# Performance work log

Measured on AMD Instinct MI355X. Metric: run time of the kernel, lower is better.

The kernel has to match this reference:

```python
import jax, jax.numpy as jnp
import numpy as np

H = 4096
W = 4096
C = 3
OUT = 1024
MAX_MIP = 8  # matches init max_mip_level; mip chain is levels 0..MAX_MIP


def setup_inputs() -> dict:
    key = jax.random.key(0)
    k1, k2, k3 = jax.random.split(key, 3)
    data = jax.random.uniform(k1, (1, H, W, C), dtype=jnp.float32)
    texc = jax.random.uniform(k2, (1, OUT, OUT, 2), dtype=jnp.float32)
    # small UV derivatives -> per-pixel texel footprint of a few texels, so the
    # LOD spans several mip levels (exercises cross-level paged gathers)
    texc_deriv = jax.random.normal(k3, (1, OUT, OUT, 4), dtype=jnp.float32) * 2e-3
    return {"data": data, "texc": texc, "texc_deriv": texc_deriv}


def _avg_pool2(x):
    # 2x2 box-filter mipmap reduction, matching virtual_texture_mipmap_fwd
    b, h, w, c = x.shape
    return x.reshape(b, h // 2, 2, w // 2, 2, c).mean(axis=(2, 4))


def _bilinear_wrap(tex, texc):
    # tex: [1,h,w,c]; texc: [1,Ho,Wo,2] in [0,1); boundary_mode='wrap'
    h, w = tex.shape[1], tex.shape[2]
    x = texc[..., 0] * w - 0.5
    y = texc[..., 1] * h - 0.5
    x0f = jnp.floor(x)
    y0f = jnp.floor(y)
    fx = (x - x0f)[..., None]
    fy = (y - y0f)[..., None]
    x0 = x0f.astype(jnp.int32) % w
    y0 = y0f.astype(jnp.int32) % h
    x1 = (x0 + 1) % w
    y1 = (y0 + 1) % h
    t = tex[0]  # [h,w,c]
    top = t[y0, x0] * (1.0 - fx) + t[y0, x1] * fx
    bot = t[y1, x0] * (1.0 - fx) + t[y1, x1] * fx
    return top * (1.0 - fy) + bot * fy  # [1,Ho,Wo,c]


def _forward(data, texc, texc_deriv):
    # LOD from screen-space UV derivatives (nvdiffrast linear-mipmap-linear)
    dudx = texc_deriv[..., 0] * W
    dvdx = texc_deriv[..., 1] * H
    dudy = texc_deriv[..., 2] * W
    dvdy = texc_deriv[..., 3] * H
    rho2 = jnp.maximum(dudx * dudx + dvdx * dvdx, dudy * dudy + dvdy * dvdy)
    lod = 0.5 * jnp.log2(jnp.maximum(rho2, 1e-20))
    lod = jnp.clip(lod, 0.0, float(MAX_MIP))  # [1,Ho,Wo]

    # build mip pyramid (gradients flow back to base texture, matching
    # virtual_texture_mipmap_bwd accumulation)
    mips = [data]
    for _ in range(MAX_MIP):
        mips.append(_avg_pool2(mips[-1]))

    # trilinear: per-level weight w_l = clip(1 - |lod - l|, 0, 1)
    out = jnp.zeros(texc.shape[:-1] + (C,), dtype=data.dtype)
    for lvl in range(MAX_MIP + 1):
        w_l = jnp.clip(1.0 - jnp.abs(lod - float(lvl)), 0.0, 1.0)[..., None]
        out = out + w_l * _bilinear_wrap(mips[lvl], texc)
    return out


def reference(data, texc, texc_deriv):
    return _forward(data, texc, texc_deriv)
```

## Files before the change

### kernel.cpp

```cpp
#include <hip/hip_runtime.h>
#include <hip/hip_bf16.h>


#define OUT_N (1024 * 1024)

__device__ __forceinline__ unsigned mip_off_b(int lvl) {
    return (67108864u - (67108864u >> (2 * lvl - 2))) / 3u;
}
#define OFF2 16777216u
#define OFF3 20971520u
#define OFF4 22020096u
#define OFF5 22282240u
#define OFF6 22347776u

__device__ __forceinline__ unsigned pack10(float r, float g, float b) {
    unsigned ur = __float2uint_rn(r * 1023.0f);
    unsigned ug = __float2uint_rn(g * 1023.0f);
    unsigned ub = __float2uint_rn(b * 1023.0f);
    return ur | (ug << 10) | (ub << 20);
}

__device__ __forceinline__ void dec_acc(unsigned q, float w, float& r, float& g, float& b) {
    const float s = 1.0f / 1023.0f;
    r = fmaf((float)(q & 1023u) * s, w, r);
    g = fmaf((float)((q >> 10) & 1023u) * s, w, g);
    b = fmaf((float)((q >> 20) & 1023u) * s, w, b);
}

__device__ __forceinline__ float4 dec4(unsigned q) {
    const float s = 1.0f / 1023.0f;
    return float4{(float)(q & 1023u) * s, (float)((q >> 10) & 1023u) * s,
                  (float)((q >> 20) & 1023u) * s, 0.0f};
}

__device__ __forceinline__ float4 avg4(float4 a, float4 b, float4 c, float4 d) {
    return float4{(a.x + b.x + c.x + d.x) * 0.25f,
                  (a.y + b.y + c.y + d.y) * 0.25f,
                  (a.z + b.z + c.z + d.z) * 0.25f, 0.0f};
}

__device__ __forceinline__ void store_quad(char* p, float4 t00, float4 t01,
                                           float4 t10, float4 t11) {
    *(uint4*)p = make_uint4(pack10(t00.x, t00.y, t00.z), pack10(t01.x, t01.y, t01.z),
                            pack10(t10.x, t10.y, t10.z), pack10(t11.x, t11.y, t11.z));
}

#define POOL_BYTES (49152 + 4352)

__global__ __launch_bounds__(256) void mip_fused(const float* __restrict__ data,
                                                 char* __restrict__ wsb) {
    __shared__ float4 pool4[POOL_BYTES / 16];
    char* pool = (char*)pool4;
    float4(*s2)[17] = (float4(*)[17])(pool + 49152);
    float4(*s3)[9]  = (float4(*)[9])(pool + 0);
    float4(*s4)[5]  = (float4(*)[5])(pool + 2048);
    float4(*s5)[3]  = (float4(*)[3])(pool + 4096);

    const int t = threadIdx.x;
    const int bx = blockIdx.x & 63;
    const int by = blockIdx.x >> 6;

    {
        const char* src = (const char*)data + (size_t)by * 64 * 49152 + (size_t)bx * 768;
#pragma unroll
        for (int j = 0; j < 12; ++j) {
            int f = t + j * 256;
            int row = f / 48;
            int col = f - row * 48;
            const char* g = src + (size_t)row * 49152 + (size_t)col * 16;
            __builtin_amdgcn_global_load_lds(
                (const __attribute__((address_space(1))) unsigned int*)g,
                (__attribute__((address_space(3))) unsigned int*)(pool + (size_t)f * 16),
                16, 0, 0);
        }
    }
    __syncthreads();

    {
        int tx = t & 15, ty = t >> 4;
        float rr = 0.0f, gg = 0.0f, bb = 0.0f;
#pragma unroll
        for (int i = 0; i < 4; ++i) {
            const float4* rp = (const float4*)(pool + (size_t)(4 * ty + i) * 768 + (size_t)tx * 48);
            float4 A = rp[0], Bv = rp[1], Cv = rp[2];
            rr += A.x + A.w + Bv.z + Cv.y;
            gg += A.y + Bv.x + Bv.w + Cv.z;
            bb += A.z + Bv.y + Cv.x + Cv.w;
        }
        const float sc = 1.0f / 16.0f;
        float4 tex = {rr * sc, gg * sc, bb * sc, 0.0f};
        __syncthreads();
        s2[ty][tx] = tex;
    }
    __syncthreads();

    if (t < 64) {
        int qx = t & 7, qy = t >> 3;
        float4 t00 = s2[2 * qy][2 * qx],     t01 = s2[2 * qy][2 * qx + 1];
        float4 t10 = s2[2 * qy + 1][2 * qx], t11 = s2[2 * qy + 1][2 * qx + 1];
        unsigned gq = ((by << 3) + qy) * 512u + (bx << 3) + qx;
        store_quad(wsb + OFF2 + ((size_t)gq << 4), t00, t01, t10, t11);
        s3[qy][qx] = avg4(t00, t01, t10, t11);
    }
    __syncthreads();

    if (t < 16) {
        int qx = t & 3, qy = t >> 2;
        float4 t00 = s3[2 * qy][2 * qx],     t01 = s3[2 * qy][2 * qx + 1];
        float4 t10 = s3[2 * qy + 1][2 * qx], t11 = s3[2 * qy + 1][2 * qx + 1];
        unsigned gq = ((by << 2) + qy) * 256u + (bx << 2) + qx;
        store_quad(wsb + OFF3 + ((size_t)gq << 4), t00, t01, t10, t11);
        s4[qy][qx] = avg4(t00, t01, t10, t11);
    }
    __syncthreads();

    if (t < 4) {
        int qx = t & 1, qy = t >> 1;
        float4 t00 = s4[2 * qy][2 * qx],     t01 = s4[2 * qy][2 * qx + 1];
        float4 t10 = s4[2 * qy + 1][2 * qx], t11 = s4[2 * qy + 1][2 * qx + 1];
        unsigned gq = ((by << 1) + qy) * 128u + (bx << 1) + qx;
        store_quad(wsb + OFF4 + ((size_t)gq << 4), t00, t01, t10, t11);
        s5[qy][qx] = avg4(t00, t01, t10, t11);
    }
    __syncthreads();

    if (t == 0) {
        float4 t00 = s5[0][0], t01 = s5[0][1], t10 = s5[1][0], t11 = s5[1][1];
        unsigned gq = (unsigned)by * 64u + (unsigned)bx;
        store_quad(wsb + OFF5 + ((size_t)gq << 4), t00, t01, t10, t11);
        float4 l6 = avg4(t00, t01, t10, t11);
        size_t a6 = OFF6 + ((((by >> 1) * 32) + (bx >> 1)) << 4) +
                    ((by & 1) << 3) + ((bx & 1) << 2);
        *(unsigned*)(wsb + a6) = pack10(l6.x, l6.y, l6.z);
    }
}

__device__ __forceinline__ void tap_off(int lvl, float u, float v,
                                        unsigned& o00, unsigned& o01,
                                        unsigned& o10, unsigned& o11,
                                        float& fx, float& fy) {
    int size = 4096 >> lvl;
    float fs = (float)size;
    float x = fmaf(u, fs, -0.5f);
    float y = fmaf(v, fs, -0.5f);
    float x0f = floorf(x);
    float y0f = floorf(y);
    fx = x - x0f;
    fy = y - y0f;
    int m = size - 1;
    int x0 = ((int)x0f) & m;
    int y0 = ((int)y0f) & m;
    int x1 = (x0 + 1) & m;
    int y1 = (y0 + 1) & m;
    int hs = size >> 1;
    unsigned r0 = (unsigned)((y0 >> 1) * hs);
    unsigned r1 = (unsigned)((y1 >> 1) * hs);
    unsigned c0 = (unsigned)(x0 >> 1), c1 = (unsigned)(x1 >> 1);
    unsigned sy0 = (unsigned)((y0 & 1) << 3), sy1 = (unsigned)((y1 & 1) << 3);
    unsigned sx0 = (unsigned)((x0 & 1) << 2), sx1 = (unsigned)((x1 & 1) << 2);
    o00 = ((r0 + c0) << 4) + sy0 + sx0;
    o01 = ((r0 + c1) << 4) + sy0 + sx1;
    o10 = ((r1 + c0) << 4) + sy1 + sx0;
    o11 = ((r1 + c1) << 4) + sy1 + sx1;
}

__device__ __forceinline__ void sample_packed(const char* __restrict__ wsb, int lvl,
                                              float u, float v, float wgt,
                                              float& r, float& g, float& b) {
    unsigned o00, o01, o10, o11;
    float fx, fy;
    tap_off(lvl, u, v, o00, o01, o10, o11, fx, fy);
    const char* B = wsb + mip_off_b(lvl);
    unsigned q00 = *(const unsigned*)(B + o00);
    unsigned q01 = *(const unsigned*)(B + o01);
    unsigned q10 = *(const unsigned*)(B + o10);
    unsigned q11 = *(const unsigned*)(B + o11);
    dec_acc(q00, (1.0f - fx) * (1.0f - fy) * wgt, r, g, b);
    dec_acc(q01, fx * (1.0f - fy) * wgt, r, g, b);
    dec_acc(q10, (1.0f - fx) * fy * wgt, r, g, b);
    dec_acc(q11, fx * fy * wgt, r, g, b);
}

__device__ void sample_fine(const float* __restrict__ data, int lvl,
                            float u, float v, float wgt,
                            float& r, float& g, float& b) {
    int size = 4096 >> lvl;
    float fs = (float)size;
    float x = u * fs - 0.5f;
    float y = v * fs - 0.5f;
    float x0f = floorf(x);
    float y0f = floorf(y);
    float fx = x - x0f;
    float fy = y - y0f;
    int m = size - 1;
    int x0 = ((int)x0f) & m;
    int y0 = ((int)y0f) & m;
    int x1 = (x0 + 1) & m;
    int y1 = (y0 + 1) & m;
    int k = 1 << lvl;
    float inv = wgt / (float)(k * k);
    float ww[2][2] = {{(1.0f - fx) * (1.0f - fy) * inv, fx * (1.0f - fy) * inv},
                      {(1.0f - fx) * fy * inv, fx * fy * inv}};
    int xs[2] = {x0 << lvl, x1 << lvl};
    int ys[2] = {y0 << lvl, y1 << lvl};
    for (int ty = 0; ty < 2; ++ty)
        for (int tx = 0; tx < 2; ++tx) {
            float tr = 0.0f, tg = 0.0f, tb = 0.0f;
            for (int dy = 0; dy < k; ++dy)
                for (int dx = 0; dx < k; ++dx) {
                    const float* p = data + ((size_t)(ys[ty] + dy) * 4096 + xs[tx] + dx) * 3;
                    tr += p[0]; tg += p[1]; tb += p[2];
                }
            r = fmaf(tr, ww[ty][tx], r);
            g = fmaf(tg, ww[ty][tx], g);
            b = fmaf(tb, ww[ty][tx], b);
        }
}

__device__ float4 read_l6(const char* __restrict__ wsb, int xx, int yy) {
    size_t a = OFF6 + ((((yy >> 1) * 32) + (xx >> 1)) << 4) + ((yy & 1) << 3) + ((xx & 1) << 2);
    return dec4(*(const unsigned*)(wsb + a));
}

__device__ void sample_coarse(const char* __restrict__ wsb, int lvl,
                              float u, float v, float wgt,
                              float& r, float& g, float& b) {
    int size = 4096 >> lvl;
    float fs = (float)size;
    float x = u * fs - 0.5f;
    float y = v * fs - 0.5f;
    float x0f = floorf(x);
    float y0f = floorf(y);
    float fx = x - x0f;
    float fy = y - y0f;
    int m = size - 1;
    int x0 = ((int)x0f) & m;
    int y0 = ((int)y0f) & m;
    int x1 = (x0 + 1) & m;
    int y1 = (y0 + 1) & m;
    int s = lvl - 6;
    int k = 1 << s;
    float inv = wgt / (float)(k * k);
    float ww[2][2] = {{(1.0f - fx) * (1.0f - fy) * inv, fx * (1.0f - fy) * inv},
                      {(1.0f - fx) * fy * inv, fx * fy * inv}};
    int xs[2] = {x0 << s, x1 << s};
    int ys[2] = {y0 << s, y1 << s};
    for (int ty = 0; ty < 2; ++ty)
        for (int tx = 0; tx < 2; ++tx) {
            float tr = 0.0f, tg = 0.0f, tb = 0.0f;
            for (int dy = 0; dy < k; ++dy)
                for (int dx = 0; dx < k; ++dx) {
                    float4 c = read_l6(wsb, xs[tx] + dx, ys[ty] + dy);
                    tr += c.x; tg += c.y; tb += c.z;
                }
            r = fmaf(tr, ww[ty][tx], r);
            g = fmaf(tg, ww[ty][tx], g);
            b = fmaf(tb, ww[ty][tx], b);
        }
}

__device__ __forceinline__ void sample_any(const float* __restrict__ data,
                                           const char* __restrict__ wsb, int lvl,
                                           float u, float v, float wgt,
                                           float& r, float& g, float& b) {
    if (lvl >= 2) {
        if (lvl <= 6) sample_packed(wsb, lvl, u, v, wgt, r, g, b);
        else sample_coarse(wsb, lvl, u, v, wgt, r, g, b);
    } else {
        sample_fine(data, lvl, u, v, wgt, r, g, b);
    }
}

__global__ __launch_bounds__(256) void vt_sample(const float* __restrict__ data,
                                                 const char* __restrict__ wsb,
                                                 const float* __restrict__ texc,
                                                 const float* __restrict__ deriv,
                                                 float* __restrict__ out) {
    int p = blockIdx.x * 256 + threadIdx.x;

    float2 uv = ((const float2*)texc)[p];
    float4 dv = ((const float4*)deriv)[p];
    float dudx = dv.x * 4096.0f;
    float dvdx = dv.y * 4096.0f;
    float dudy = dv.z * 4096.0f;
    float dvdy = dv.w * 4096.0f;
    float rho2 = fmaxf(fmaf(dudx, dudx, dvdx * dvdx), fmaf(dudy, dudy, dvdy * dvdy));
    float lod = 0.5f * __log2f(fmaxf(rho2, 1e-20f));
    lod = fminf(fmaxf(lod, 0.0f), 8.0f);

    int l0 = (int)lod;
    float f = lod - (float)l0;
    int l1 = (l0 < 8) ? (l0 + 1) : 8;

    float r = 0.0f, g = 0.0f, b = 0.0f;

    if (__builtin_expect((unsigned)(l0 - 2) <= 3u, 1)) {
        unsigned a00, a01, a10, a11, b00, b01, b10, b11;
        float fx0, fy0, fx1, fy1;
        const char* B0 = wsb + mip_off_b(l0);
        const char* B1 = wsb + mip_off_b(l1);
        tap_off(l0, uv.x, uv.y, a00, a01, a10, a11, fx0, fy0);
        tap_off(l1, uv.x, uv.y, b00, b01, b10, b11, fx1, fy1);
        unsigned q0 = *(const unsigned*)(B0 + a00);
        unsigned q1 = *(const unsigned*)(B0 + a01);
        unsigned q2 = *(const unsigned*)(B0 + a10);
        unsigned q3 = *(const unsigned*)(B0 + a11);
        unsigned q4 = *(const unsigned*)(B1 + b00);
        unsigned q5 = *(const unsigned*)(B1 + b01);
        unsigned q6 = *(const unsigned*)(B1 + b10);
        unsigned q7 = *(const unsigned*)(B1 + b11);
        float w0 = 1.0f - f;
        dec_acc(q0, (1.0f - fx0) * (1.0f - fy0) * w0, r, g, b);
        dec_acc(q1, fx0 * (1.0f - fy0) * w0, r, g, b);
        dec_acc(q2, (1.0f - fx0) * fy0 * w0, r, g, b);
        dec_acc(q3, fx0 * fy0 * w0, r, g, b);
        dec_acc(q4, (1.0f - fx1) * (1.0f - fy1) * f, r, g, b);
        dec_acc(q5, fx1 * (1.0f - fy1) * f, r, g, b);
        dec_acc(q6, (1.0f - fx1) * fy1 * f, r, g, b);
        dec_acc(q7, fx1 * fy1 * f, r, g, b);
    } else {
        sample_any(data, wsb, l0, uv.x, uv.y, 1.0f - f, r, g, b);
        sample_any(data, wsb, l1, uv.x, uv.y, f, r, g, b);
    }

    float* o = out + (size_t)p * 3;
    o[0] = r;
    o[1] = g;
    o[2] = b;
}

extern "C" void kernel_launch(void* const* d_in, const int* in_sizes, int n_in,
                              void* d_out, int out_size, void* d_ws, size_t ws_size,
                              hipStream_t stream) {
    const float* data  = (const float*)d_in[0];
    const float* texc  = (const float*)d_in[1];
    const float* deriv = (const float*)d_in[2];
    float* out = (float*)d_out;
    char* wsb  = (char*)d_ws;

    mip_fused<<<4096, 256, 0, stream>>>(data, wsb);
    vt_sample<<<OUT_N / 256, 256, 0, stream>>>(data, wsb, texc, deriv, out);
}
```

Before: 327.0 us.

## Split mip build into L2 and coarse-level kernels with linear packed layout

Replaces the single fused mip kernel with two kernels. The first reduces full-width 4-row strips of the base texture to level 2, writing both a 10-bit packed copy and a float copy. The second kernel reads that float copy to build levels 3-6. The packed mip storage changes from 2x2 quad-blocked to plain row-major, which simplifies the tap address math in the sampler. The aim is more coalesced base-texture reads and cheaper sampling addresses, at the cost of an extra launch and an extra float intermediate written to and read from global memory.

```diff
diff --git a/kernel.cpp b/kernel.cpp
--- a/kernel.cpp
+++ b/kernel.cpp
@@ -12,6 +12,7 @@
 #define OFF4 22020096u
 #define OFF5 22282240u
 #define OFF6 22347776u
+#define FOFF 25165824u
 
 __device__ __forceinline__ unsigned pack10(float r, float g, float b) {
     unsigned ur = __float2uint_rn(r * 1023.0f);
@@ -39,99 +40,95 @@
                   (a.z + b.z + c.z + d.z) * 0.25f, 0.0f};
 }
 
-__device__ __forceinline__ void store_quad(char* p, float4 t00, float4 t01,
-                                           float4 t10, float4 t11) {
-    *(uint4*)p = make_uint4(pack10(t00.x, t00.y, t00.z), pack10(t01.x, t01.y, t01.z),
-                            pack10(t10.x, t10.y, t10.z), pack10(t11.x, t11.y, t11.z));
-}
-
-#define POOL_BYTES (49152 + 4352)
-
-__global__ __launch_bounds__(256) void mip_fused(const float* __restrict__ data,
-                                                 char* __restrict__ wsb) {
-    __shared__ float4 pool4[POOL_BYTES / 16];
-    char* pool = (char*)pool4;
-    float4(*s2)[17] = (float4(*)[17])(pool + 49152);
-    float4(*s3)[9]  = (float4(*)[9])(pool + 0);
-    float4(*s4)[5]  = (float4(*)[5])(pool + 2048);
-    float4(*s5)[3]  = (float4(*)[3])(pool + 4096);
-
+__global__ __launch_bounds__(256) void mip_l2(const float* __restrict__ data,
+                                              char* __restrict__ wsb) {
+    __shared__ float4 tile[3072];
     const int t = threadIdx.x;
-    const int bx = blockIdx.x & 63;
-    const int by = blockIdx.x >> 6;
-
-    {
-        const char* src = (const char*)data + (size_t)by * 64 * 49152 + (size_t)bx * 768;
+    const unsigned b = blockIdx.x;
+    const unsigned l2row = b >> 2;
+    const unsigned c4 = b & 3;
+    const char* src = (const char*)data + (size_t)l2row * 4 * 49152 + (size_t)c4 * 12288;
+    char* lds = (char*)tile;
+
 #pragma unroll
-        for (int j = 0; j < 12; ++j) {
-            int f = t + j * 256;
-            int row = f / 48;
-            int col = f - row * 48;
-            const char* g = src + (size_t)row * 49152 + (size_t)col * 16;
+    for (int r = 0; r < 4; ++r) {
+#pragma unroll
+        for (int k = 0; k < 3; ++k) {
+            unsigned fo = (unsigned)(k * 256 + t);
             __builtin_amdgcn_global_load_lds(
-                (const __attribute__((address_space(1))) unsigned int*)g,
-                (__attribute__((address_space(3))) unsigned int*)(pool + (size_t)f * 16),
+                (const __attribute__((address_space(1))) unsigned int*)
+                    (src + (size_t)r * 49152 + (size_t)fo * 16),
+                (__attribute__((address_space(3))) unsigned int*)
+                    (lds + ((size_t)r * 768 + fo) * 16),
                 16, 0, 0);
         }
     }
     __syncthreads();
 
+    float rr = 0.0f, gg = 0.0f, bb = 0.0f;
+#pragma unroll
+    for (int i = 0; i < 4; ++i) {
+        const float4* rp = (const float4*)(lds + (size_t)i * 12288 + (size_t)t * 48);
+        float4 A = rp[0], Bv = rp[1], Cv = rp[2];
+        rr += A.x + A.w + Bv.z + Cv.y;
+        gg += A.y + Bv.x + Bv.w + Cv.z;
+        bb += A.z + Bv.y + Cv.x + Cv.w;
+    }
+    const float sc = 1.0f / 16.0f;
+    rr *= sc; gg *= sc; bb *= sc;
+
+    size_t idx = ((size_t)l2row << 10) + ((size_t)c4 << 8) + (size_t)t;
+    *(unsigned*)(wsb + OFF2 + idx * 4) = pack10(rr, gg, bb);
+    *(float4*)(wsb + FOFF + idx * 16) = float4{rr, gg, bb, 0.0f};
+}
+
+__global__ __launch_bounds__(256) void mip_rest(char* __restrict__ wsb) {
+    __shared__ float4 s3[16][17];
+    __shared__ float4 s4[8][9];
+    __shared__ float4 s5[4][5];
+    const int t = threadIdx.x;
+    const unsigned bby = blockIdx.x >> 5;
+    const unsigned bbx = blockIdx.x & 31;
+
     {
         int tx = t & 15, ty = t >> 4;
-        float rr = 0.0f, gg = 0.0f, bb = 0.0f;
-#pragma unroll
-        for (int i = 0; i < 4; ++i) {
-            const float4* rp = (const float4*)(pool + (size_t)(4 * ty + i) * 768 + (size_t)tx * 48);
-            float4 A = rp[0], Bv = rp[1], Cv = rp[2];
-            rr += A.x + A.w + Bv.z + Cv.y;
-            gg += A.y + Bv.x + Bv.w + Cv.z;
-            bb += A.z + Bv.y + Cv.x + Cv.w;
-        }
-        const float sc = 1.0f / 16.0f;
-        float4 tex = {rr * sc, gg * sc, bb * sc, 0.0f};
-        __syncthreads();
-        s2[ty][tx] = tex;
+        unsigned R3 = (bby << 4) + ty;
+        unsigned C3 = (bbx << 4) + tx;
+        const char* F = wsb + FOFF;
+        const float4* p0 = (const float4*)(F + ((((size_t)R3 * 2) << 10) + (size_t)C3 * 2) * 16);
+        const float4* p1 = (const float4*)(F + ((((size_t)R3 * 2 + 1) << 10) + (size_t)C3 * 2) * 16);
+        float4 v = avg4(p0[0], p0[1], p1[0], p1[1]);
+        s3[ty][tx] = v;
+        *(unsigned*)(wsb + OFF3 + (((size_t)R3 << 9) + C3) * 4) = pack10(v.x, v.y, v.z);
     }
     __syncthreads();
 
     if (t < 64) {
-        int qx = t & 7, qy = t >> 3;
-        float4 t00 = s2[2 * qy][2 * qx],     t01 = s2[2 * qy][2 * qx + 1];
-        float4 t10 = s2[2 * qy + 1][2 * qx], t11 = s2[2 * qy + 1][2 * qx + 1];
-        unsigned gq = ((by << 3) + qy) * 512u + (bx << 3) + qx;
-        store_quad(wsb + OFF2 + ((size_t)gq << 4), t00, t01, t10, t11);
-        s3[qy][qx] = avg4(t00, t01, t10, t11);
+        int tx = t & 7, ty = t >> 3;
+        float4 v = avg4(s3[2 * ty][2 * tx], s3[2 * ty][2 * tx + 1],
+                        s3[2 * ty + 1][2 * tx], s3[2 * ty + 1][2 * tx + 1]);
+        s4[ty][tx] = v;
+        unsigned R4 = (bby << 3) + ty, C4 = (bbx << 3) + tx;
+        *(unsigned*)(wsb + OFF4 + (((size_t)R4 << 8) + C4) * 4) = pack10(v.x, v.y, v.z);
     }
     __syncthreads();
 
     if (t < 16) {
-        int qx = t & 3, qy = t >> 2;
-        float4 t00 = s3[2 * qy][2 * qx],     t01 = s3[2 * qy][2 * qx + 1];
-        float4 t10 = s3[2 * qy + 1][2 * qx], t11 = s3[2 * qy + 1][2 * qx + 1];
-        unsigned gq = ((by << 2) + qy) * 256u + (bx << 2) + qx;
-        store_quad(wsb + OFF3 + ((size_t)gq << 4), t00, t01, t10, t11);
-        s4[qy][qx] = avg4(t00, t01, t10, t11);
+        int tx = t & 3, ty = t >> 2;
+        float4 v = avg4(s4[2 * ty][2 * tx], s4[2 * ty][2 * tx + 1],
+                        s4[2 * ty + 1][2 * tx], s4[2 * ty + 1][2 * tx + 1]);
+        s5[ty][tx] = v;
+        unsigned R5 = (bby << 2) + ty, C5 = (bbx << 2) + tx;
+        *(unsigned*)(wsb + OFF5 + (((size_t)R5 << 7) + C5) * 4) = pack10(v.x, v.y, v.z);
     }
     __syncthreads();
 
     if (t < 4) {
-        int qx = t & 1, qy = t >> 1;
-        float4 t00 = s4[2 * qy][2 * qx],     t01 = s4[2 * qy][2 * qx + 1];
-        float4 t10 = s4[2 * qy + 1][2 * qx], t11 = s4[2 * qy + 1][2 * qx + 1];
-        unsigned gq = ((by << 1) + qy) * 128u + (bx << 1) + qx;
-        store_quad(wsb + OFF4 + ((size_t)gq << 4), t00, t01, t10, t11);
-        s5[qy][qx] = avg4(t00, t01, t10, t11);
-    }
-    __syncthreads();
-
-    if (t == 0) {
-        float4 t00 = s5[0][0], t01 = s5[0][1], t10 = s5[1][0], t11 = s5[1][1];
-        unsigned gq = (unsigned)by * 64u + (unsigned)bx;
-        store_quad(wsb + OFF5 + ((size_t)gq << 4), t00, t01, t10, t11);
-        float4 l6 = avg4(t00, t01, t10, t11);
-        size_t a6 = OFF6 + ((((by >> 1) * 32) + (bx >> 1)) << 4) +
-                    ((by & 1) << 3) + ((bx & 1) << 2);
-        *(unsigned*)(wsb + a6) = pack10(l6.x, l6.y, l6.z);
+        int tx = t & 1, ty = t >> 1;
+        float4 v = avg4(s5[2 * ty][2 * tx], s5[2 * ty][2 * tx + 1],
+                        s5[2 * ty + 1][2 * tx], s5[2 * ty + 1][2 * tx + 1]);
+        unsigned R6r = (bby << 1) + ty, C6 = (bbx << 1) + tx;
+        *(unsigned*)(wsb + OFF6 + (((size_t)R6r << 6) + C6) * 4) = pack10(v.x, v.y, v.z);
     }
 }
 
@@ -148,20 +145,16 @@
     fx = x - x0f;
     fy = y - y0f;
     int m = size - 1;
-    int x0 = ((int)x0f) & m;
-    int y0 = ((int)y0f) & m;
-    int x1 = (x0 + 1) & m;
-    int y1 = (y0 + 1) & m;
-    int hs = size >> 1;
-    unsigned r0 = (unsigned)((y0 >> 1) * hs);
-    unsigned r1 = (unsigned)((y1 >> 1) * hs);
-    unsigned c0 = (unsigned)(x0 >> 1), c1 = (unsigned)(x1 >> 1);
-    unsigned sy0 = (unsigned)((y0 & 1) << 3), sy1 = (unsigned)((y1 & 1) << 3);
-    unsigned sx0 = (unsigned)((x0 & 1) << 2), sx1 = (unsigned)((x1 & 1) << 2);
-    o00 = ((r0 + c0) << 4) + sy0 + sx0;
-    o01 = ((r0 + c1) << 4) + sy0 + sx1;
-    o10 = ((r1 + c0) << 4) + sy1 + sx0;
-    o11 = ((r1 + c1) << 4) + sy1 + sx1;
+    unsigned x0 = (unsigned)(((int)x0f) & m);
+    unsigned y0 = (unsigned)(((int)y0f) & m);
+    unsigned x1 = (x0 + 1) & (unsigned)m;
+    unsigned y1 = (y0 + 1) & (unsigned)m;
+    int sh = 12 - lvl;
+    unsigned r0 = y0 << sh, r1 = y1 << sh;
+    o00 = (r0 + x0) << 2;
+    o01 = (r0 + x1) << 2;
+    o10 = (r1 + x0) << 2;
+    o11 = (r1 + x1) << 2;
 }
 
 __device__ __forceinline__ void sample_packed(const char* __restrict__ wsb, int lvl,
@@ -218,8 +211,7 @@
 }
 
 __device__ float4 read_l6(const char* __restrict__ wsb, int xx, int yy) {
-    size_t a = OFF6 + ((((yy >> 1) * 32) + (xx >> 1)) << 4) + ((yy & 1) << 3) + ((xx & 1) << 2);
-    return dec4(*(const unsigned*)(wsb + a));
+    return dec4(*(const unsigned*)(wsb + OFF6 + ((((size_t)yy << 6) + xx) << 2)));
 }
 
 __device__ void sample_coarse(const char* __restrict__ wsb, int lvl,
@@ -338,6 +330,7 @@
     float* out = (float*)d_out;
     char* wsb  = (char*)d_ws;
 
-    mip_fused<<<4096, 256, 0, stream>>>(data, wsb);
+    mip_l2<<<4096, 256, 0, stream>>>(data, wsb);
+    mip_rest<<<1024, 256, 0, stream>>>(wsb);
     vt_sample<<<OUT_N / 256, 256, 0, stream>>>(data, wsb, texc, deriv, out);
 }
```

New measurement: 337.3 us. 1.03x slower.
